# Kernel optimization log

Measured on AMD Instinct MI355X. Metric: run time of the kernel, lower is better.

The kernel has to match this reference:

```python
import jax, jax.numpy as jnp
import numpy as np

B, S, D_IN = 2, 2048, 1024
H, D_HEAD = 16, 64  # n_heads, output_dim == hidden_size


def setup_inputs() -> dict:
    key = jax.random.key(0)
    k1, k2, k3 = jax.random.split(key, 3)
    x = jax.random.normal(k1, (B, S, D_IN), dtype=jnp.float32)
    # he_normal-ish init: std = sqrt(2 / fan_in)
    kernel = jax.random.normal(k2, (3, H, D_IN, D_HEAD), dtype=jnp.float32) * np.float32(np.sqrt(2.0 / D_IN))
    WO = jax.random.normal(k3, (1, H * D_HEAD, D_IN), dtype=jnp.float32) * np.float32(np.sqrt(2.0 / (H * D_HEAD)))
    return {"x": x, "kernel": kernel, "WO": WO}


def reference(x, kernel, WO):
    b, s, _ = x.shape
    h, d = kernel.shape[1], kernel.shape[3]
    # K.dot(x, kernel[i]): contract x last axis with kernel axis -2 -> (B,S,H,d);
    # original then permutes to (B,H,S,d); fuse both into one einsum.
    q = jnp.einsum('bsm,hmd->bhsd', x, kernel[0])
    k = jnp.einsum('bsm,hmd->bhsd', x, kernel[1])
    v = jnp.einsum('bsm,hmd->bhsd', x, kernel[2])
    # scores scaled by /output_dim /hidden_size /n_heads (output_dim==hidden_size)
    scale = jnp.float32(1.0 / (d * d * h))
    scores = jnp.einsum('bhsd,bhtd->bhst', q, k) * scale  # (B,H,S,S)
    attn = jax.nn.softmax(scores, axis=-1)
    out = jnp.einsum('bhst,bhtd->bhsd', attn, v)          # (B,H,S,d)
    # original: permute to (B,S,d,H) then reshape to (B,S,d*H) -> d-major, H-minor
    out = jnp.transpose(out, (0, 2, 3, 1)).reshape(b, s, d * h)
    out = jnp.einsum('bsf,fm->bsm', out, WO[0])           # (B,S,D_IN)
    return out
```

## Files before the change

### kernel.cpp

```cpp
#include <hip/hip_runtime.h>
#include <hip/hip_bf16.h>


typedef unsigned short u16;
typedef __attribute__((ext_vector_type(8))) short bf16x8;
typedef __attribute__((ext_vector_type(4))) short bf16x4;
typedef __attribute__((ext_vector_type(4))) float f32x4;
typedef __attribute__((ext_vector_type(4))) unsigned short u16x4;
typedef __attribute__((ext_vector_type(8))) unsigned short u16x8;
typedef __attribute__((ext_vector_type(4))) unsigned int u32x4;

#define SCALE 1.52587890625e-05f

__device__ __forceinline__ u16 f2bf(float f) {
  unsigned int u = __float_as_uint(f);
  return (u16)((u + 0x7FFFu + ((u >> 16) & 1u)) >> 16);
}
__device__ __forceinline__ float bf2f(u16 v) {
  return __uint_as_float(((unsigned int)v) << 16);
}

__device__ __forceinline__ f32x4 mfma16(bf16x8 a, bf16x8 b, f32x4 c) {
  return __builtin_amdgcn_mfma_f32_16x16x32_bf16(a, b, c, 0, 0, 0);
}

__device__ __forceinline__ void gl_lds16(const u16* g, u16* l) {
  __builtin_amdgcn_global_load_lds((const __attribute__((address_space(1))) void*)g,
                                   (__attribute__((address_space(3))) void*)l, 16, 0, 0);
}

__global__ void split_f32(const float* __restrict__ x, u16* __restrict__ hi,
                          u16* __restrict__ lo, int n4) {
  int i = blockIdx.x * 256 + threadIdx.x;
  if (i >= n4) return;
  float4 v = ((const float4*)x)[i];
  float vv[4] = {v.x, v.y, v.z, v.w};
  u16x4 h, l;
#pragma unroll
  for (int j = 0; j < 4; ++j) {
    u16 hb = f2bf(vv[j]);
    h[j] = hb;
    l[j] = f2bf(vv[j] - bf2f(hb));
  }
  ((u16x4*)hi)[i] = h;
  ((u16x4*)lo)[i] = l;
}

__global__ void prep_w(const float* __restrict__ w, u16* __restrict__ bhi,
                       u16* __restrict__ blo) {
  __shared__ float t[64 * 65];
  int mt = blockIdx.x, th = blockIdx.y;
  float scl = (th < 16) ? SCALE : 1.0f;
  int tid = threadIdx.x;
  for (int i = 0; i < 16; ++i) {
    int idx = tid + i * 256;
    int ms = idx >> 6, d = idx & 63;
    t[d * 65 + ms] = w[(size_t)(th * 1024 + mt * 64 + ms) * 64 + d];
  }
  __syncthreads();
  for (int i = 0; i < 16; ++i) {
    int idx = tid + i * 256;
    int ds = idx >> 6, mm = idx & 63;
    float v = t[ds * 65 + mm] * scl;
    size_t o = (size_t)(th * 64 + ds) * 1024 + mt * 64 + mm;
    u16 hb = f2bf(v);
    bhi[o] = hb;
    blo[o] = f2bf(v - bf2f(hb));
  }
}

__global__ void prep_wo(const float* __restrict__ wo, u16* __restrict__ bhi,
                        u16* __restrict__ blo) {
  __shared__ float t[64 * 65];
  int mt = blockIdx.x, kt = blockIdx.y;
  int tid = threadIdx.x;
  for (int i = 0; i < 16; ++i) {
    int idx = tid + i * 256;
    int d = idx >> 6, mm = idx & 63;
    t[mm * 65 + d] = wo[(size_t)(d * 16 + kt) * 1024 + mt * 64 + mm];
  }
  __syncthreads();
  for (int i = 0; i < 16; ++i) {
    int idx = tid + i * 256;
    int mr = idx >> 6, dc = idx & 63;
    float v = t[mr * 65 + dc];
    size_t o = (size_t)(mt * 64 + mr) * 1024 + kt * 64 + dc;
    u16 hb = f2bf(v);
    bhi[o] = hb;
    blo[o] = f2bf(v - bf2f(hb));
  }
}

__global__ __launch_bounds__(256, 2) void gemm_qkv(
    const u16* __restrict__ Ah_g, const u16* __restrict__ Al_g,
    const u16* __restrict__ Bh_g, const u16* __restrict__ Bl_g,
    u16* __restrict__ Qb, u16* __restrict__ Kb, u16* __restrict__ Vb) {
  __shared__ __align__(16) u16 Ah[128 * 32];
  __shared__ __align__(16) u16 Al[128 * 32];
  __shared__ __align__(16) u16 Bh[128 * 32];
  __shared__ __align__(16) u16 Bl[128 * 32];
  int tid = threadIdx.x;
  int lane = tid & 63;
  int l15 = lane & 15, g = lane >> 4;
  int wv = tid >> 6, wm = wv >> 1, wn = wv & 1;
  int m0 = blockIdx.x * 128, n0 = blockIdx.y * 128;
  bool full = (n0 >= 2048);

  f32x4 acc[4][4];
#pragma unroll
  for (int i = 0; i < 4; ++i)
#pragma unroll
    for (int j = 0; j < 4; ++j) acc[i][j] = (f32x4){0.f, 0.f, 0.f, 0.f};

  int c0 = tid, c1 = tid + 256;
  int r0 = c0 >> 2, o0 = (c0 & 3) * 8;
  int r1 = c1 >> 2, o1 = (c1 & 3) * 8;
  int wb0 = (tid & 192) * 8, wb1 = ((tid & 192) + 256) * 8;

  for (int kk = 0; kk < 32; ++kk) {
    int k0 = kk * 32;
    __syncthreads();
    gl_lds16(Ah_g + (size_t)(m0 + r0) * 1024 + k0 + o0, &Ah[wb0]);
    gl_lds16(Ah_g + (size_t)(m0 + r1) * 1024 + k0 + o1, &Ah[wb1]);
    gl_lds16(Bh_g + (size_t)(n0 + r0) * 1024 + k0 + o0, &Bh[wb0]);
    gl_lds16(Bh_g + (size_t)(n0 + r1) * 1024 + k0 + o1, &Bh[wb1]);
    if (full) {
      gl_lds16(Al_g + (size_t)(m0 + r0) * 1024 + k0 + o0, &Al[wb0]);
      gl_lds16(Al_g + (size_t)(m0 + r1) * 1024 + k0 + o1, &Al[wb1]);
      gl_lds16(Bl_g + (size_t)(n0 + r0) * 1024 + k0 + o0, &Bl[wb0]);
      gl_lds16(Bl_g + (size_t)(n0 + r1) * 1024 + k0 + o1, &Bl[wb1]);
    }
    __syncthreads();

    bf16x8 fa_h[4], fa_l[4], fb_h[4], fb_l[4];
#pragma unroll
    for (int mi = 0; mi < 4; ++mi) {
      int off = (wm * 64 + mi * 16 + l15) * 64 + g * 16;
      fa_h[mi] = *(const bf16x8*)((const char*)Ah + off);
      if (full) fa_l[mi] = *(const bf16x8*)((const char*)Al + off);
    }
#pragma unroll
    for (int ni = 0; ni < 4; ++ni) {
      int off = (wn * 64 + ni * 16 + l15) * 64 + g * 16;
      fb_h[ni] = *(const bf16x8*)((const char*)Bh + off);
      if (full) fb_l[ni] = *(const bf16x8*)((const char*)Bl + off);
    }
    if (full) {
#pragma unroll
      for (int mi = 0; mi < 4; ++mi)
#pragma unroll
        for (int ni = 0; ni < 4; ++ni) {
          acc[mi][ni] = mfma16(fa_h[mi], fb_h[ni], acc[mi][ni]);
          acc[mi][ni] = mfma16(fa_h[mi], fb_l[ni], acc[mi][ni]);
          acc[mi][ni] = mfma16(fa_l[mi], fb_h[ni], acc[mi][ni]);
        }
    } else {
#pragma unroll
      for (int mi = 0; mi < 4; ++mi)
#pragma unroll
        for (int ni = 0; ni < 4; ++ni)
          acc[mi][ni] = mfma16(fa_h[mi], fb_h[ni], acc[mi][ni]);
    }
  }

  if (full) {
#pragma unroll
    for (int mi = 0; mi < 4; ++mi)
#pragma unroll
      for (int ni = 0; ni < 4; ++ni) {
        int n = n0 + wn * 64 + ni * 16 + l15;
        int d = n & 63, h = (n >> 6) & 15;
        int s0 = m0 + wm * 64 + mi * 16 + g * 4;
        int b = s0 >> 11, s = s0 & 2047;
        u16x4 vv;
#pragma unroll
        for (int rr = 0; rr < 4; ++rr) vv[rr] = f2bf(acc[mi][ni][rr]);
        *(u16x4*)(Vb + (size_t)((b * 16 + h) * 64 + d) * 2048 + s) = vv;
      }
  } else {
#pragma unroll
    for (int mi = 0; mi < 4; ++mi)
#pragma unroll
      for (int ni = 0; ni < 4; ++ni)
#pragma unroll
        for (int rr = 0; rr < 4; ++rr) {
          int m = m0 + wm * 64 + mi * 16 + g * 4 + rr;
          int n = n0 + wn * 64 + ni * 16 + l15;
          int th = n >> 6, d = n & 63;
          int t = th >> 4, h = th & 15;
          int b = m >> 11, s = m & 2047;
          u16* ob = t ? Kb : Qb;
          ob[(size_t)((b * 16 + h) * 2048 + s) * 64 + d] = f2bf(acc[mi][ni][rr]);
        }
  }
}

__global__ __launch_bounds__(256, 2) void gemm_c(
    const u16* __restrict__ Ah_g, const u16* __restrict__ Al_g,
    const u16* __restrict__ Bh_g, const u16* __restrict__ Bl_g,
    float* __restrict__ Cf) {
  __shared__ __align__(16) u16 Ah[128 * 32];
  __shared__ __align__(16) u16 Al[128 * 32];
  __shared__ __align__(16) u16 Bh[64 * 32];
  __shared__ __align__(16) u16 Bl[64 * 32];
  int tid = threadIdx.x;
  int lane = tid & 63;
  int l15 = lane & 15, g = lane >> 4;
  int wv = tid >> 6, wm = wv >> 1, wn = wv & 1;
  int m0 = blockIdx.x * 128, n0 = blockIdx.y * 64;

  f32x4 acc[4][2];
#pragma unroll
  for (int i = 0; i < 4; ++i)
#pragma unroll
    for (int j = 0; j < 2; ++j) acc[i][j] = (f32x4){0.f, 0.f, 0.f, 0.f};

  int r0 = tid >> 2, o0 = (tid & 3) * 8;
  int r1 = r0 + 64;
  int wb0 = (tid & 192) * 8, wb1 = ((tid & 192) + 256) * 8;

  for (int kk = 0; kk < 32; ++kk) {
    int k0 = kk * 32;
    __syncthreads();
    gl_lds16(Ah_g + (size_t)(m0 + r0) * 1024 + k0 + o0, &Ah[wb0]);
    gl_lds16(Ah_g + (size_t)(m0 + r1) * 1024 + k0 + o0, &Ah[wb1]);
    gl_lds16(Al_g + (size_t)(m0 + r0) * 1024 + k0 + o0, &Al[wb0]);
    gl_lds16(Al_g + (size_t)(m0 + r1) * 1024 + k0 + o0, &Al[wb1]);
    gl_lds16(Bh_g + (size_t)(n0 + r0) * 1024 + k0 + o0, &Bh[wb0]);
    gl_lds16(Bl_g + (size_t)(n0 + r0) * 1024 + k0 + o0, &Bl[wb0]);
    __syncthreads();

    bf16x8 fa_h[4], fa_l[4], fb_h[2], fb_l[2];
#pragma unroll
    for (int mi = 0; mi < 4; ++mi) {
      int off = (wm * 64 + mi * 16 + l15) * 64 + g * 16;
      fa_h[mi] = *(const bf16x8*)((const char*)Ah + off);
      fa_l[mi] = *(const bf16x8*)((const char*)Al + off);
    }
#pragma unroll
    for (int ni = 0; ni < 2; ++ni) {
      int off = (wn * 32 + ni * 16 + l15) * 64 + g * 16;
      fb_h[ni] = *(const bf16x8*)((const char*)Bh + off);
      fb_l[ni] = *(const bf16x8*)((const char*)Bl + off);
    }
#pragma unroll
    for (int mi = 0; mi < 4; ++mi)
#pragma unroll
      for (int ni = 0; ni < 2; ++ni) {
        acc[mi][ni] = mfma16(fa_h[mi], fb_h[ni], acc[mi][ni]);
        acc[mi][ni] = mfma16(fa_h[mi], fb_l[ni], acc[mi][ni]);
        acc[mi][ni] = mfma16(fa_l[mi], fb_h[ni], acc[mi][ni]);
      }
  }

#pragma unroll
  for (int mi = 0; mi < 4; ++mi)
#pragma unroll
    for (int ni = 0; ni < 2; ++ni)
#pragma unroll
      for (int rr = 0; rr < 4; ++rr) {
        int m = m0 + wm * 64 + mi * 16 + g * 4 + rr;
        int n = n0 + wn * 32 + ni * 16 + l15;
        Cf[(size_t)m * 1024 + n] = acc[mi][ni][rr];
      }
}

__global__ void colsum_v(const u16* __restrict__ Vt, float* __restrict__ cs) {
  int blk = blockIdx.x;
  int bh = blk >> 3, dg = blk & 7;
  int tid = threadIdx.x;
  int ld = tid >> 5, l32 = tid & 31;
  int d = dg * 8 + ld;
  const u16x8* row = (const u16x8*)(Vt + (size_t)(bh * 64 + d) * 2048);
  float s = 0.f;
#pragma unroll
  for (int i = 0; i < 8; ++i) {
    u16x8 v = row[l32 + i * 32];
#pragma unroll
    for (int j = 0; j < 8; ++j) s += bf2f(v[j]);
  }
  s += __shfl_xor(s, 1);
  s += __shfl_xor(s, 2);
  s += __shfl_xor(s, 4);
  s += __shfl_xor(s, 8);
  s += __shfl_xor(s, 16);
  if (l32 == 0) cs[bh * 64 + d] = s;
}

__global__ __launch_bounds__(256, 4) void attn(
    const u16* __restrict__ Qb, const u16* __restrict__ Kb,
    const u16* __restrict__ Vt, const float* __restrict__ csum,
    u16* __restrict__ AOhi, u16* __restrict__ AOlo) {
  __shared__ __align__(16) u16 Kl[128 * 64];
  __shared__ __align__(16) u16 Vl[64 * 128];
  int bid = blockIdx.x;
  int id = bid >> 3;
  int bh = (bid & 7) * 4 + (id >> 5);
  int qt = id & 31;
  int tid = threadIdx.x, lane = tid & 63, w = tid >> 6;
  int l15 = lane & 15, g = lane >> 4;
  const u16* Qg = Qb + (size_t)bh * 2048 * 64;
  const u16* Kg = Kb + (size_t)bh * 2048 * 64;
  const u16* Vg = Vt + (size_t)bh * 64 * 2048;
  int q_base = qt * 64 + w * 16;
  int wbase = tid & 192;

  bf16x8 qf[2];
#pragma unroll
  for (int ds = 0; ds < 2; ++ds)
    qf[ds] = *(const bf16x8*)(Qg + (size_t)(q_base + l15) * 64 + ds * 32 + g * 8);

  f32x4 acc_e[4], acc_l;
#pragma unroll
  for (int i = 0; i < 4; ++i) acc_e[i] = (f32x4){0.f, 0.f, 0.f, 0.f};
  acc_l = (f32x4){0.f, 0.f, 0.f, 0.f};
  const f32x4 zf = (f32x4){0.f, 0.f, 0.f, 0.f};
  bf16x8 ones;
#pragma unroll
  for (int j = 0; j < 8; ++j) ones[j] = (short)0x3F80;

  union PU { u32x4 u; bf16x8 b; };

  for (int tt0 = 0; tt0 < 16; ++tt0) {
    int t0 = tt0 * 128;
    __syncthreads();
#pragma unroll
    for (int i = 0; i < 4; ++i) {
      int c = tid + i * 256;
      int krow = c >> 3, kblk = c & 7;
      gl_lds16(Kg + (size_t)(t0 + krow) * 64 + ((kblk ^ (krow & 7)) * 8),
               &Kl[(wbase + i * 256) * 8]);
      int vd = c >> 4, vsb = c & 15;
      gl_lds16(Vg + (size_t)vd * 2048 + t0 + ((vsb ^ (vd & 7)) * 8),
               &Vl[(wbase + i * 256) * 8]);
    }
    __syncthreads();

    f32x4 sc[8];
    __builtin_amdgcn_s_setprio(1);
#pragma unroll
    for (int tt = 0; tt < 8; ++tt) {
      int row = tt * 16 + l15;
      int off0 = row * 128 + (((g ^ (row & 7)) << 4));
      int off1 = row * 128 + ((((4 + g) ^ (row & 7)) << 4));
      bf16x8 kf0 = *(const bf16x8*)((const char*)Kl + off0);
      bf16x8 kf1 = *(const bf16x8*)((const char*)Kl + off1);
      sc[tt] = mfma16(kf0, qf[0], zf);
      sc[tt] = mfma16(kf1, qf[1], sc[tt]);
    }
    __builtin_amdgcn_s_setprio(0);

    PU pe[4];
#pragma unroll
    for (int ks = 0; ks < 4; ++ks) {
#pragma unroll
      for (int blk = 0; blk < 2; ++blk) {
        f32x4 s4 = sc[ks * 2 + blk];
        float e0 = __builtin_fmaf(0.5f * s4[0], s4[0], s4[0]);
        float e1 = __builtin_fmaf(0.5f * s4[1], s4[1], s4[1]);
        float e2 = __builtin_fmaf(0.5f * s4[2], s4[2], s4[2]);
        float e3 = __builtin_fmaf(0.5f * s4[3], s4[3], s4[3]);
        pe[ks].u[blk * 2] = __builtin_amdgcn_perm(
            __float_as_uint(e1), __float_as_uint(e0), 0x07060302u);
        pe[ks].u[blk * 2 + 1] = __builtin_amdgcn_perm(
            __float_as_uint(e3), __float_as_uint(e2), 0x07060302u);
      }
      acc_l = mfma16(pe[ks].b, ones, acc_l);
    }

    int xm = (l15 & 7) << 4;
    const char* Vrow = (const char*)Vl + l15 * 256;
    __builtin_amdgcn_s_setprio(1);
#pragma unroll
    for (int ks = 0; ks < 4; ++ks) {
      int t0a = (ks * 64 + 8 * g) ^ xm;
      int t1a = (ks * 64 + 32 + 8 * g) ^ xm;
#pragma unroll
      for (int dt = 0; dt < 4; ++dt) {
        bf16x4 lo = *(const bf16x4*)(Vrow + dt * 4096 + t0a);
        bf16x4 hi = *(const bf16x4*)(Vrow + dt * 4096 + t1a);
        bf16x8 vf = (bf16x8){lo[0], lo[1], lo[2], lo[3],
                             hi[0], hi[1], hi[2], hi[3]};
        acc_e[dt] = mfma16(pe[ks].b, vf, acc_e[dt]);
      }
    }
    __builtin_amdgcn_s_setprio(0);
  }

  float linv[4];
#pragma unroll
  for (int r = 0; r < 4; ++r) linv[r] = 1.0f / (2048.0f + acc_l[r]);

  int b = bh >> 4, h = bh & 15;
#pragma unroll
  for (int dt = 0; dt < 4; ++dt) {
    float cv = csum[bh * 64 + dt * 16 + l15];
#pragma unroll
    for (int r = 0; r < 4; ++r) {
      int s = q_base + g * 4 + r;
      int d = dt * 16 + l15;
      float o = (cv + acc_e[dt][r]) * linv[r];
      u16 hv = f2bf(o);
      size_t ao = ((size_t)(b * 2048 + s) * 16 + h) * 64 + d;
      AOhi[ao] = hv;
      AOlo[ao] = f2bf(o - bf2f(hv));
    }
  }
}

extern "C" void kernel_launch(void* const* d_in, const int* in_sizes, int n_in,
                              void* d_out, int out_size, void* d_ws,
                              size_t ws_size, hipStream_t stream) {
  const float* x = (const float*)d_in[0];
  const float* krn = (const float*)d_in[1];
  const float* wo = (const float*)d_in[2];
  float* out = (float*)d_out;

  u16* p = (u16*)d_ws;
  u16* Xhi = p;   p += 4096 * 1024;
  u16* Xlo = p;   p += 4096 * 1024;
  u16* Wthi = p;  p += 3072 * 1024;
  u16* Wtlo = p;  p += 3072 * 1024;
  u16* WOthi = p; p += 1024 * 1024;
  u16* WOtlo = p; p += 1024 * 1024;
  u16* Qb = p;    p += 4194304;
  u16* Kb = p;    p += 4194304;
  u16* Vtb = p;   p += 4194304;
  u16* AOhi = p;  p += 4194304;
  u16* AOlo = p;  p += 4194304;
  float* Csum = (float*)p;

  split_f32<<<4096, 256, 0, stream>>>(x, Xhi, Xlo, 1048576);
  prep_w<<<dim3(16, 48), 256, 0, stream>>>(krn, Wthi, Wtlo);
  prep_wo<<<dim3(16, 16), 256, 0, stream>>>(wo, WOthi, WOtlo);
  gemm_qkv<<<dim3(32, 24), 256, 0, stream>>>(Xhi, Xlo, Wthi, Wtlo, Qb, Kb, Vtb);
  colsum_v<<<256, 256, 0, stream>>>(Vtb, Csum);
  attn<<<1024, 256, 0, stream>>>(Qb, Kb, Vtb, Csum, AOhi, AOlo);
  gemm_c<<<dim3(32, 16), 256, 0, stream>>>(AOhi, AOlo, WOthi, WOtlo, out);
}
```

Before: 241.2 us.

## Fuse prep kernels, fold V column-sum into QKV GEMM, reorder block schedule

Merges the three input/weight preparation kernels into one launch and removes the separate V column-sum kernel. The column sums are now accumulated with atomics in the QKV GEMM epilogue, which needs a memset of the sum buffer first. The QKV GEMM moves to a 1D grid that schedules the heavier 3-pass V tiles first and gives the Q/K tiles a 64-wide K step per barrier, halving their synchronisations. This trades fewer launches and less V re-reading for atomic contention and float-order nondeterminism in the sums.

```diff
diff --git a/kernel.cpp b/kernel.cpp
--- a/kernel.cpp
+++ b/kernel.cpp
@@ -29,82 +29,90 @@
                                    (__attribute__((address_space(3))) void*)l, 16, 0, 0);
 }
 
-__global__ void split_f32(const float* __restrict__ x, u16* __restrict__ hi,
-                          u16* __restrict__ lo, int n4) {
-  int i = blockIdx.x * 256 + threadIdx.x;
-  if (i >= n4) return;
-  float4 v = ((const float4*)x)[i];
-  float vv[4] = {v.x, v.y, v.z, v.w};
-  u16x4 h, l;
-#pragma unroll
-  for (int j = 0; j < 4; ++j) {
-    u16 hb = f2bf(vv[j]);
-    h[j] = hb;
-    l[j] = f2bf(vv[j] - bf2f(hb));
-  }
-  ((u16x4*)hi)[i] = h;
-  ((u16x4*)lo)[i] = l;
-}
-
-__global__ void prep_w(const float* __restrict__ w, u16* __restrict__ bhi,
-                       u16* __restrict__ blo) {
+__global__ __launch_bounds__(256) void prep_all(
+    const float* __restrict__ x, const float* __restrict__ krn,
+    const float* __restrict__ wo, u16* __restrict__ Xhi, u16* __restrict__ Xlo,
+    u16* __restrict__ Wthi, u16* __restrict__ Wtlo, u16* __restrict__ WOthi,
+    u16* __restrict__ WOtlo) {
   __shared__ float t[64 * 65];
-  int mt = blockIdx.x, th = blockIdx.y;
-  float scl = (th < 16) ? SCALE : 1.0f;
-  int tid = threadIdx.x;
-  for (int i = 0; i < 16; ++i) {
-    int idx = tid + i * 256;
-    int ms = idx >> 6, d = idx & 63;
-    t[d * 65 + ms] = w[(size_t)(th * 1024 + mt * 64 + ms) * 64 + d];
-  }
-  __syncthreads();
-  for (int i = 0; i < 16; ++i) {
-    int idx = tid + i * 256;
-    int ds = idx >> 6, mm = idx & 63;
-    float v = t[ds * 65 + mm] * scl;
-    size_t o = (size_t)(th * 64 + ds) * 1024 + mt * 64 + mm;
-    u16 hb = f2bf(v);
-    bhi[o] = hb;
-    blo[o] = f2bf(v - bf2f(hb));
-  }
-}
-
-__global__ void prep_wo(const float* __restrict__ wo, u16* __restrict__ bhi,
-                        u16* __restrict__ blo) {
-  __shared__ float t[64 * 65];
-  int mt = blockIdx.x, kt = blockIdx.y;
-  int tid = threadIdx.x;
-  for (int i = 0; i < 16; ++i) {
-    int idx = tid + i * 256;
-    int d = idx >> 6, mm = idx & 63;
-    t[mm * 65 + d] = wo[(size_t)(d * 16 + kt) * 1024 + mt * 64 + mm];
-  }
-  __syncthreads();
-  for (int i = 0; i < 16; ++i) {
-    int idx = tid + i * 256;
-    int mr = idx >> 6, dc = idx & 63;
-    float v = t[mr * 65 + dc];
-    size_t o = (size_t)(mt * 64 + mr) * 1024 + kt * 64 + dc;
-    u16 hb = f2bf(v);
-    bhi[o] = hb;
-    blo[o] = f2bf(v - bf2f(hb));
+  int bid = blockIdx.x, tid = threadIdx.x;
+  if (bid < 4096) {
+    int i = bid * 256 + tid;
+    float4 v = ((const float4*)x)[i];
+    float vv[4] = {v.x, v.y, v.z, v.w};
+    u16x4 h, l;
+#pragma unroll
+    for (int j = 0; j < 4; ++j) {
+      u16 hb = f2bf(vv[j]);
+      h[j] = hb;
+      l[j] = f2bf(vv[j] - bf2f(hb));
+    }
+    ((u16x4*)Xhi)[i] = h;
+    ((u16x4*)Xlo)[i] = l;
+  } else if (bid < 4864) {
+    int q = bid - 4096;
+    int mt = q & 15, th = q >> 4;
+    float scl = (th < 16) ? SCALE : 1.0f;
+    for (int i = 0; i < 16; ++i) {
+      int idx = tid + i * 256;
+      int ms = idx >> 6, d = idx & 63;
+      t[d * 65 + ms] = krn[(size_t)(th * 1024 + mt * 64 + ms) * 64 + d];
+    }
+    __syncthreads();
+    for (int i = 0; i < 16; ++i) {
+      int idx = tid + i * 256;
+      int ds = idx >> 6, mm = idx & 63;
+      float v = t[ds * 65 + mm] * scl;
+      size_t o = (size_t)(th * 64 + ds) * 1024 + mt * 64 + mm;
+      u16 hb = f2bf(v);
+      Wthi[o] = hb;
+      Wtlo[o] = f2bf(v - bf2f(hb));
+    }
+  } else {
+    int q = bid - 4864;
+    int mt = q & 15, kt = q >> 4;
+    for (int i = 0; i < 16; ++i) {
+      int idx = tid + i * 256;
+      int d = idx >> 6, mm = idx & 63;
+      t[mm * 65 + d] = wo[(size_t)(d * 16 + kt) * 1024 + mt * 64 + mm];
+    }
+    __syncthreads();
+    for (int i = 0; i < 16; ++i) {
+      int idx = tid + i * 256;
+      int mr = idx >> 6, dc = idx & 63;
+      float v = t[mr * 65 + dc];
+      size_t o = (size_t)(mt * 64 + mr) * 1024 + kt * 64 + dc;
+      u16 hb = f2bf(v);
+      WOthi[o] = hb;
+      WOtlo[o] = f2bf(v - bf2f(hb));
+    }
   }
 }
 
 __global__ __launch_bounds__(256, 2) void gemm_qkv(
     const u16* __restrict__ Ah_g, const u16* __restrict__ Al_g,
     const u16* __restrict__ Bh_g, const u16* __restrict__ Bl_g,
-    u16* __restrict__ Qb, u16* __restrict__ Kb, u16* __restrict__ Vb) {
+    u16* __restrict__ Qb, u16* __restrict__ Kb, u16* __restrict__ Vb,
+    float* __restrict__ cs) {
   __shared__ __align__(16) u16 Ah[128 * 32];
   __shared__ __align__(16) u16 Al[128 * 32];
   __shared__ __align__(16) u16 Bh[128 * 32];
   __shared__ __align__(16) u16 Bl[128 * 32];
+  int bid = blockIdx.x;
+  bool full = (bid < 256);
+  int m0, n0;
+  if (full) {
+    m0 = (bid >> 3) * 128;
+    n0 = 2048 + (bid & 7) * 128;
+  } else {
+    int q = bid - 256;
+    m0 = (q >> 4) * 128;
+    n0 = (q & 15) * 128;
+  }
   int tid = threadIdx.x;
   int lane = tid & 63;
   int l15 = lane & 15, g = lane >> 4;
   int wv = tid >> 6, wm = wv >> 1, wn = wv & 1;
-  int m0 = blockIdx.x * 128, n0 = blockIdx.y * 128;
-  bool full = (n0 >= 2048);
 
   f32x4 acc[4][4];
 #pragma unroll
@@ -117,35 +125,33 @@
   int r1 = c1 >> 2, o1 = (c1 & 3) * 8;
   int wb0 = (tid & 192) * 8, wb1 = ((tid & 192) + 256) * 8;
 
-  for (int kk = 0; kk < 32; ++kk) {
-    int k0 = kk * 32;
-    __syncthreads();
-    gl_lds16(Ah_g + (size_t)(m0 + r0) * 1024 + k0 + o0, &Ah[wb0]);
-    gl_lds16(Ah_g + (size_t)(m0 + r1) * 1024 + k0 + o1, &Ah[wb1]);
-    gl_lds16(Bh_g + (size_t)(n0 + r0) * 1024 + k0 + o0, &Bh[wb0]);
-    gl_lds16(Bh_g + (size_t)(n0 + r1) * 1024 + k0 + o1, &Bh[wb1]);
-    if (full) {
+  if (full) {
+    for (int kk = 0; kk < 32; ++kk) {
+      int k0 = kk * 32;
+      __syncthreads();
+      gl_lds16(Ah_g + (size_t)(m0 + r0) * 1024 + k0 + o0, &Ah[wb0]);
+      gl_lds16(Ah_g + (size_t)(m0 + r1) * 1024 + k0 + o1, &Ah[wb1]);
+      gl_lds16(Bh_g + (size_t)(n0 + r0) * 1024 + k0 + o0, &Bh[wb0]);
+      gl_lds16(Bh_g + (size_t)(n0 + r1) * 1024 + k0 + o1, &Bh[wb1]);
       gl_lds16(Al_g + (size_t)(m0 + r0) * 1024 + k0 + o0, &Al[wb0]);
       gl_lds16(Al_g + (size_t)(m0 + r1) * 1024 + k0 + o1, &Al[wb1]);
       gl_lds16(Bl_g + (size_t)(n0 + r0) * 1024 + k0 + o0, &Bl[wb0]);
       gl_lds16(Bl_g + (size_t)(n0 + r1) * 1024 + k0 + o1, &Bl[wb1]);
-    }
-    __syncthreads();
-
-    bf16x8 fa_h[4], fa_l[4], fb_h[4], fb_l[4];
-#pragma unroll
-    for (int mi = 0; mi < 4; ++mi) {
-      int off = (wm * 64 + mi * 16 + l15) * 64 + g * 16;
-      fa_h[mi] = *(const bf16x8*)((const char*)Ah + off);
-      if (full) fa_l[mi] = *(const bf16x8*)((const char*)Al + off);
-    }
-#pragma unroll
-    for (int ni = 0; ni < 4; ++ni) {
-      int off = (wn * 64 + ni * 16 + l15) * 64 + g * 16;
-      fb_h[ni] = *(const bf16x8*)((const char*)Bh + off);
-      if (full) fb_l[ni] = *(const bf16x8*)((const char*)Bl + off);
-    }
-    if (full) {
+      __syncthreads();
+
+      bf16x8 fa_h[4], fa_l[4], fb_h[4], fb_l[4];
+#pragma unroll
+      for (int mi = 0; mi < 4; ++mi) {
+        int off = (wm * 64 + mi * 16 + l15) * 64 + g * 16;
+        fa_h[mi] = *(const bf16x8*)((const char*)Ah + off);
+        fa_l[mi] = *(const bf16x8*)((const char*)Al + off);
+      }
+#pragma unroll
+      for (int ni = 0; ni < 4; ++ni) {
+        int off = (wn * 64 + ni * 16 + l15) * 64 + g * 16;
+        fb_h[ni] = *(const bf16x8*)((const char*)Bh + off);
+        fb_l[ni] = *(const bf16x8*)((const char*)Bl + off);
+      }
 #pragma unroll
       for (int mi = 0; mi < 4; ++mi)
 #pragma unroll
@@ -154,30 +160,62 @@
           acc[mi][ni] = mfma16(fa_h[mi], fb_l[ni], acc[mi][ni]);
           acc[mi][ni] = mfma16(fa_l[mi], fb_h[ni], acc[mi][ni]);
         }
-    } else {
-#pragma unroll
-      for (int mi = 0; mi < 4; ++mi)
+    }
+
+    int b = m0 >> 11, h = ((n0 >> 6) + wn) & 15;
+#pragma unroll
+    for (int ni = 0; ni < 4; ++ni) {
+      int d = (wn * 64 + ni * 16 + l15) & 63;
+      float psum = 0.f;
+#pragma unroll
+      for (int mi = 0; mi < 4; ++mi) {
+        int s0 = m0 + wm * 64 + mi * 16 + g * 4;
+        int s = s0 & 2047;
+        u16x4 vv;
+#pragma unroll
+        for (int rr = 0; rr < 4; ++rr) {
+          psum += acc[mi][ni][rr];
+          vv[rr] = f2bf(acc[mi][ni][rr]);
+        }
+        *(u16x4*)(Vb + (size_t)((b * 16 + h) * 64 + d) * 2048 + s) = vv;
+      }
+      psum += __shfl_down(psum, 16);
+      psum += __shfl_down(psum, 32);
+      if (g == 0) atomicAdd(&cs[(b * 16 + h) * 64 + d], psum);
+    }
+  } else {
+    for (int kk = 0; kk < 16; ++kk) {
+      int k0 = kk * 64;
+      __syncthreads();
+      gl_lds16(Ah_g + (size_t)(m0 + r0) * 1024 + k0 + o0, &Ah[wb0]);
+      gl_lds16(Ah_g + (size_t)(m0 + r1) * 1024 + k0 + o1, &Ah[wb1]);
+      gl_lds16(Bh_g + (size_t)(n0 + r0) * 1024 + k0 + o0, &Bh[wb0]);
+      gl_lds16(Bh_g + (size_t)(n0 + r1) * 1024 + k0 + o1, &Bh[wb1]);
+      gl_lds16(Ah_g + (size_t)(m0 + r0) * 1024 + k0 + 32 + o0, &Al[wb0]);
+      gl_lds16(Ah_g + (size_t)(m0 + r1) * 1024 + k0 + 32 + o1, &Al[wb1]);
+      gl_lds16(Bh_g + (size_t)(n0 + r0) * 1024 + k0 + 32 + o0, &Bl[wb0]);
+      gl_lds16(Bh_g + (size_t)(n0 + r1) * 1024 + k0 + 32 + o1, &Bl[wb1]);
+      __syncthreads();
+
+#pragma unroll
+      for (int kh = 0; kh < 2; ++kh) {
+        const char* As = kh ? (const char*)Al : (const char*)Ah;
+        const char* Bs = kh ? (const char*)Bl : (const char*)Bh;
+        bf16x8 fa[4], fb[4];
+#pragma unroll
+        for (int mi = 0; mi < 4; ++mi)
+          fa[mi] = *(const bf16x8*)(As + (wm * 64 + mi * 16 + l15) * 64 + g * 16);
 #pragma unroll
         for (int ni = 0; ni < 4; ++ni)
-          acc[mi][ni] = mfma16(fa_h[mi], fb_h[ni], acc[mi][ni]);
-    }
-  }
-
-  if (full) {
-#pragma unroll
-    for (int mi = 0; mi < 4; ++mi)
-#pragma unroll
-      for (int ni = 0; ni < 4; ++ni) {
-        int n = n0 + wn * 64 + ni * 16 + l15;
-        int d = n & 63, h = (n >> 6) & 15;
-        int s0 = m0 + wm * 64 + mi * 16 + g * 4;
-        int b = s0 >> 11, s = s0 & 2047;
-        u16x4 vv;
-#pragma unroll
-        for (int rr = 0; rr < 4; ++rr) vv[rr] = f2bf(acc[mi][ni][rr]);
-        *(u16x4*)(Vb + (size_t)((b * 16 + h) * 64 + d) * 2048 + s) = vv;
-      }
-  } else {
+          fb[ni] = *(const bf16x8*)(Bs + (wn * 64 + ni * 16 + l15) * 64 + g * 16);
+#pragma unroll
+        for (int mi = 0; mi < 4; ++mi)
+#pragma unroll
+          for (int ni = 0; ni < 4; ++ni)
+            acc[mi][ni] = mfma16(fa[mi], fb[ni], acc[mi][ni]);
+      }
+    }
+
 #pragma unroll
     for (int mi = 0; mi < 4; ++mi)
 #pragma unroll
@@ -263,28 +301,6 @@
         int n = n0 + wn * 32 + ni * 16 + l15;
         Cf[(size_t)m * 1024 + n] = acc[mi][ni][rr];
       }
-}
-
-__global__ void colsum_v(const u16* __restrict__ Vt, float* __restrict__ cs) {
-  int blk = blockIdx.x;
-  int bh = blk >> 3, dg = blk & 7;
-  int tid = threadIdx.x;
-  int ld = tid >> 5, l32 = tid & 31;
-  int d = dg * 8 + ld;
-  const u16x8* row = (const u16x8*)(Vt + (size_t)(bh * 64 + d) * 2048);
-  float s = 0.f;
-#pragma unroll
-  for (int i = 0; i < 8; ++i) {
-    u16x8 v = row[l32 + i * 32];
-#pragma unroll
-    for (int j = 0; j < 8; ++j) s += bf2f(v[j]);
-  }
-  s += __shfl_xor(s, 1);
-  s += __shfl_xor(s, 2);
-  s += __shfl_xor(s, 4);
-  s += __shfl_xor(s, 8);
-  s += __shfl_xor(s, 16);
-  if (l32 == 0) cs[bh * 64 + d] = s;
 }
 
 __global__ __launch_bounds__(256, 4) void attn(
@@ -430,11 +446,10 @@
   u16* AOlo = p;  p += 4194304;
   float* Csum = (float*)p;
 
-  split_f32<<<4096, 256, 0, stream>>>(x, Xhi, Xlo, 1048576);
-  prep_w<<<dim3(16, 48), 256, 0, stream>>>(krn, Wthi, Wtlo);
-  prep_wo<<<dim3(16, 16), 256, 0, stream>>>(wo, WOthi, WOtlo);
-  gemm_qkv<<<dim3(32, 24), 256, 0, stream>>>(Xhi, Xlo, Wthi, Wtlo, Qb, Kb, Vtb);
-  colsum_v<<<256, 256, 0, stream>>>(Vtb, Csum);
+  hipMemsetAsync(Csum, 0, 2048 * sizeof(float), stream);
+  prep_all<<<5120, 256, 0, stream>>>(x, krn, wo, Xhi, Xlo, Wthi, Wtlo, WOthi,
+                                     WOtlo);
+  gemm_qkv<<<768, 256, 0, stream>>>(Xhi, Xlo, Wthi, Wtlo, Qb, Kb, Vtb, Csum);
   attn<<<1024, 256, 0, stream>>>(Qb, Kb, Vtb, Csum, AOhi, AOlo);
   gemm_c<<<dim3(32, 16), 256, 0, stream>>>(AOhi, AOlo, WOthi, WOtlo, out);
 }
```

New measurement: 212.1 us. -12.1%, faster.
